# Optimization experiments

Hardware: AMD Instinct MI355X
Metric: run time of the kernel (lower is better)

## Reference

```python
import jax, jax.numpy as jnp
import numpy as np

B = 8192
NUM_SAMPLES = 128
RESAMPLE_PADDING = 0.01
F32_EPS = float(np.finfo(np.float32).eps)


def lift_gaussian_diag(d, t_mean, t_var, r_var):
    # d: [B,3]; t_mean/t_var/r_var: [B,S]
    mean = d[..., None, :] * t_mean[..., None]                      # [B,S,3]
    d_mag_sq = jnp.clip(jnp.sum(d ** 2, axis=-1, keepdims=True), 1e-10)
    d_outer_diag = d ** 2
    null_outer_diag = 1.0 - d_outer_diag / d_mag_sq
    cov_diag = (t_var[..., None] * d_outer_diag[..., None, :]
                + r_var[..., None] * null_outer_diag[..., None, :])  # [B,S,3]
    return mean, cov_diag


def conical_frustum_to_gaussian(d, t0, t1, base_radius):
    # stable=True branch of the original code
    mu = (t0 + t1) / 2
    hw = (t1 - t0) / 2
    t_mean = mu + 2 * mu * hw ** 2 / (3 * mu ** 2 + hw ** 2)
    t_var = hw ** 2 / 3 - 4 / 15 * (hw ** 4 * (12 * mu ** 2 - hw ** 2)
                                    / (3 * mu ** 2 + hw ** 2) ** 2)
    r_var = base_radius ** 2 * (mu ** 2 / 4 + 5 / 12 * hw ** 2
                                - 4 / 15 * hw ** 4 / (3 * mu ** 2 + hw ** 2))
    return lift_gaussian_diag(d, t_mean, t_var, r_var)


def cast_rays(t_vals, origins, directions, radii):
    # ray_shape == 'cone', diag == True
    means, covs = conical_frustum_to_gaussian(
        directions, t_vals[..., :-1], t_vals[..., 1:], radii)
    return means + origins[..., None, :], covs


def sorted_piecewise_constant_pdf(bins, weights, num_samples):
    # randomized=False branch; faithful O(n*m) mask-based interval search
    eps = 1e-5
    weight_sum = jnp.sum(weights, axis=-1, keepdims=True)
    padding = jnp.clip(eps - weight_sum, 0)
    weights = weights + padding / weights.shape[-1]
    weight_sum = weight_sum + padding
    pdf = weights / weight_sum
    cdf = jnp.minimum(jnp.cumsum(pdf[..., :-1], axis=-1), 1.0)
    z = jnp.zeros(cdf.shape[:-1] + (1,), cdf.dtype)
    o = jnp.ones(cdf.shape[:-1] + (1,), cdf.dtype)
    cdf = jnp.concatenate([z, cdf, o], axis=-1)                      # [B, nb+1]
    u = jnp.linspace(0.0, 1.0 - F32_EPS, num_samples, dtype=cdf.dtype)
    u = jnp.broadcast_to(u, cdf.shape[:-1] + (num_samples,))         # [B, S]
    mask = u[..., None, :] >= cdf[..., :, None]                      # [B, nb+1, S]

    def find_interval(x):
        x0 = jnp.max(jnp.where(mask, x[..., None], x[..., :1, None]), axis=-2)
        x1 = jnp.min(jnp.where(~mask, x[..., None], x[..., -1:, None]), axis=-2)
        return x0, x1

    bins_g0, bins_g1 = find_interval(bins)
    cdf_g0, cdf_g1 = find_interval(cdf)
    t = jnp.clip(jnp.nan_to_num((u - cdf_g0) / (cdf_g1 - cdf_g0)), 0, 1)
    return bins_g0 + t * (bins_g1 - bins_g0)


def setup_inputs() -> dict:
    key = jax.random.key(0)
    k0, k1, k2, k3 = jax.random.split(key, 4)
    origins = jax.random.normal(k0, (B, 3), dtype=jnp.float32)
    directions = jax.random.normal(k1, (B, 3), dtype=jnp.float32)
    directions = directions / jnp.linalg.norm(directions, axis=-1, keepdims=True)
    radii = 0.001 + 0.01 * jax.random.uniform(k2, (B, 1), dtype=jnp.float32)
    near = 2.0 * jnp.ones((B, 1), dtype=jnp.float32)
    far = 6.0 * jnp.ones((B, 1), dtype=jnp.float32)
    weights = jax.random.uniform(k3, (B, NUM_SAMPLES), dtype=jnp.float32)
    return {"origins": origins, "directions": directions, "radii": radii,
            "near": near, "far": far, "weights": weights}


def reference(origins, directions, radii, near, far, weights):
    # coarse stratified sampling (randomized=False, lindisp=False)
    t = jnp.linspace(0.0, 1.0, NUM_SAMPLES + 1, dtype=jnp.float32)
    t_coarse = near * (1.0 - t) + far * t                            # [B, S+1]
    means_c, covs_c = cast_rays(t_coarse, origins, directions, radii)
    # resample_along_rays: blur weights then inverse-CDF sample
    wpad = jnp.concatenate([weights[..., :1], weights, weights[..., -1:]], axis=-1)
    wmax = jnp.maximum(wpad[..., :-1], wpad[..., 1:])
    wblur = 0.5 * (wmax[..., :-1] + wmax[..., 1:]) + RESAMPLE_PADDING
    t_fine = sorted_piecewise_constant_pdf(t_coarse, wblur, t_coarse.shape[-1])
    means_f, covs_f = cast_rays(t_fine, origins, directions, radii)
    return (t_coarse, means_c, covs_c, t_fine, means_f, covs_f)
```

## Files before the change

### kernel.cpp

```cpp
#include <hip/hip_runtime.h>


constexpr int B_RAYS = 8192;
constexpr int S      = 128;
constexpr int SP1    = 129;
constexpr float F32_EPS = 1.1920928955078125e-07f;

constexpr long long O_TC = 0;
constexpr long long O_MC = O_TC + (long long)B_RAYS * SP1;
constexpr long long O_CC = O_MC + (long long)B_RAYS * S * 3;
constexpr long long O_TF = O_CC + (long long)B_RAYS * S * 3;
constexpr long long O_MF = O_TF + (long long)B_RAYS * SP1;
constexpr long long O_CF = O_MF + (long long)B_RAYS * S * 3;

__device__ __forceinline__ float frcp(float x) { return __builtin_amdgcn_rcpf(x); }

__device__ __forceinline__ void frustum(float t0, float t1, float rad2,
                                        float& tm, float& tv, float& rv)
{
    float mu  = 0.5f * (t0 + t1);
    float hw  = 0.5f * (t1 - t0);
    float mu2 = mu * mu, hw2 = hw * hw, hw4 = hw2 * hw2;
    float den  = fmaf(3.0f, mu2, hw2);
    float rden = frcp(den);
    tm = fmaf(2.0f * mu * hw2, rden, mu);
    tv = hw2 * (1.0f / 3.0f)
       - (4.0f / 15.0f) * (hw4 * fmaf(12.0f, mu2, -hw2)) * (rden * rden);
    rv = rad2 * (0.25f * mu2 + (5.0f / 12.0f) * hw2 - (4.0f / 15.0f) * hw4 * rden);
}

__device__ __forceinline__ float sel3(int c, float x, float y, float z)
{
    return (c == 0) ? x : ((c == 1) ? y : z);
}

__global__ __launch_bounds__(256) void mipnerf_kernel(
    const float* __restrict__ origins,
    const float* __restrict__ directions,
    const float* __restrict__ radii,
    const float* __restrict__ nearp,
    const float* __restrict__ farp,
    const float* __restrict__ weights,
    float* __restrict__ out)
{
    const int tid = threadIdx.x;
    const int w   = tid >> 6;
    const int l   = tid & 63;
    const int b   = (blockIdx.x << 2) + w;

    __shared__ float2 s_ft[4][128];
    __shared__ float  s_rv[4][128];
    __shared__ float  s_cdf[4][132];
    __shared__ float  s_tf[4][132];

    const float2 wv = *reinterpret_cast<const float2*>(weights + (long long)b * S + 2*l);
    const float ox = origins[3*b+0], oy = origins[3*b+1], oz = origins[3*b+2];
    const float dx = directions[3*b+0], dy = directions[3*b+1], dz = directions[3*b+2];
    const float rad = radii[b];
    const float nv = nearp[b], fv = farp[b];

    const float rad2   = rad * rad;
    const float axx = dx*dx, ayy = dy*dy, azz = dz*dz;
    const float dmag2  = fmaxf(axx + ayy + azz, 1e-10f);
    const float rdmag2 = frcp(dmag2);
    const float nxx = 1.0f - axx * rdmag2;
    const float nyy = 1.0f - ayy * rdmag2;
    const float nzz = 1.0f - azz * rdmag2;

    auto bin = [&](int k) {
        float t = (float)k * (1.0f / 128.0f);
        return nv * (1.0f - t) + fv * t;
    };

    {
        float* ot = out + O_TC + (long long)b * SP1;
        ot[l]      = bin(l);
        ot[l + 64] = bin(l + 64);
        if (l == 0) ot[128] = bin(128);
    }

    #pragma unroll
    for (int j = 0; j < 2; ++j) {
        int i = l + 64*j;
        float tm, tv, rv;
        frustum(bin(i), bin(i + 1), rad2, tm, tv, rv);
        s_ft[w][i] = make_float2(tm, tv);
        s_rv[w][i] = rv;
    }
    __builtin_amdgcn_wave_barrier();

    auto emit_span = [&](int m, float* __restrict__ om, float* __restrict__ oc) {
        int k0 = m + m / 3;
        int r  = 4*m - 3*k0;
        float2 fA = s_ft[w][k0], fB = s_ft[w][k0 + 1];
        float  rA = s_rv[w][k0], rB = s_rv[w][k0 + 1];
        float4 mv, cv;
        #pragma unroll
        for (int e = 0; e < 4; ++e) {
            int  rc   = r + e;
            bool useB = rc >= 3;
            int  c    = useB ? rc - 3 : rc;
            float tm = useB ? fB.x : fA.x;
            float tv = useB ? fB.y : fA.y;
            float rv = useB ? rB   : rA;
            (&mv.x)[e] = sel3(c, dx, dy, dz) * tm + sel3(c, ox, oy, oz);
            (&cv.x)[e] = tv * sel3(c, axx, ayy, azz) + rv * sel3(c, nxx, nyy, nzz);
        }
        *reinterpret_cast<float4*>(om + 4*m) = mv;
        *reinterpret_cast<float4*>(oc + 4*m) = cv;
    };

    {
        float* om = out + O_MC + (long long)b * 384;
        float* oc = out + O_CC + (long long)b * 384;
        emit_span(l, om, oc);
        if (l < 32) emit_span(l + 64, om, oc);
    }

    float wprev = __shfl_up(wv.y, 1);   if (l == 0)  wprev = wv.x;
    float wnext = __shfl_down(wv.x, 1); if (l == 63) wnext = wv.y;
    float m0 = fmaxf(wprev, wv.x), m1 = fmaxf(wv.x, wv.y), m2 = fmaxf(wv.y, wnext);
    float wb0 = 0.5f * (m0 + m1) + 0.01f;
    float wb1 = 0.5f * (m1 + m2) + 0.01f;

    float ps   = wb0 + wb1;
    float incl = ps;
    #pragma unroll
    for (int off = 1; off < 64; off <<= 1) {
        float y = __shfl_up(incl, off);
        if (l >= off) incl += y;
    }
    float total = __shfl(incl, 63);
    float pad   = fmaxf(1e-5f - total, 0.0f);
    float wstot = total + pad;
    float inv   = frcp(wstot);
    float padk  = pad * (1.0f / 128.0f);
    float excl  = incl - ps;

    float c1 = fminf((excl + wb0 + (float)(2*l + 1) * padk) * inv, 1.0f);
    float c2 = fminf((incl        + (float)(2*l + 2) * padk) * inv, 1.0f);
    s_cdf[w][2*l + 1] = c1;
    s_cdf[w][2*l + 2] = (l == 63) ? 1.0f : c2;
    if (l == 0) s_cdf[w][0] = 0.0f;
    __builtin_amdgcn_wave_barrier();

    const float ustep = (1.0f - F32_EPS) * (1.0f / 128.0f);
    const float u0 = (float)l * ustep;
    const float u1 = (float)(l + 64) * ustep;
    const float u2 = 128.0f * ustep;
    int lo0 = 0, hi0 = 128, lo1 = 0, hi1 = 128, lo2 = 0, hi2 = 128;
    #pragma unroll
    for (int it = 0; it < 7; ++it) {
        int q0 = (lo0 + hi0) >> 1, q1 = (lo1 + hi1) >> 1, q2 = (lo2 + hi2) >> 1;
        float a0 = s_cdf[w][q0], a1 = s_cdf[w][q1], a2 = s_cdf[w][q2];
        if (a0 <= u0) lo0 = q0; else hi0 = q0;
        if (a1 <= u1) lo1 = q1; else hi1 = q1;
        if (a2 <= u2) lo2 = q2; else hi2 = q2;
    }
    auto interp = [&](float u, int lo) {
        float c0  = s_cdf[w][lo], cg1 = s_cdf[w][lo + 1];
        float tt  = (u - c0) * frcp(cg1 - c0);
        if (!(tt == tt)) tt = 0.0f;
        tt = fminf(fmaxf(tt, 0.0f), 1.0f);
        float b0 = bin(lo);
        return fmaf(tt, bin(lo + 1) - b0, b0);
    };
    float tf0 = interp(u0, lo0);
    float tf1 = interp(u1, lo1);
    float tf2 = interp(u2, lo2);
    {
        float* ot = out + O_TF + (long long)b * SP1;
        s_tf[w][l]      = tf0;  ot[l]      = tf0;
        s_tf[w][l + 64] = tf1;  ot[l + 64] = tf1;
        if (l == 0) { s_tf[w][128] = tf2; ot[128] = tf2; }
    }
    __builtin_amdgcn_wave_barrier();

    #pragma unroll
    for (int j = 0; j < 2; ++j) {
        int i = l + 64*j;
        float tm, tv, rv;
        frustum(s_tf[w][i], s_tf[w][i + 1], rad2, tm, tv, rv);
        s_ft[w][i] = make_float2(tm, tv);
        s_rv[w][i] = rv;
    }
    __builtin_amdgcn_wave_barrier();

    {
        float* om = out + O_MF + (long long)b * 384;
        float* oc = out + O_CF + (long long)b * 384;
        emit_span(l, om, oc);
        if (l < 32) emit_span(l + 64, om, oc);
    }
}

extern "C" void kernel_launch(void* const* d_in, const int* in_sizes, int n_in,
                              void* d_out, int out_size, void* d_ws, size_t ws_size,
                              hipStream_t stream)
{
    const float* origins    = (const float*)d_in[0];
    const float* directions = (const float*)d_in[1];
    const float* radii      = (const float*)d_in[2];
    const float* nearp      = (const float*)d_in[3];
    const float* farp       = (const float*)d_in[4];
    const float* weights    = (const float*)d_in[5];
    float* out = (float*)d_out;

    mipnerf_kernel<<<B_RAYS / 4, 256, 0, stream>>>(
        origins, directions, radii, nearp, farp, weights, out);
}
```

Measured before the change: 17.95 us.

## Replace binary CDF search with scatter of interval payloads and DPP scans

Each CDF segment computes which uniform sample indices fall in it and writes a packed payload (cdf start, width, bin endpoints) into shared memory, so each sample reads one entry instead of running a 7-step binary search. The wave shuffles and prefix scan are swapped for DPP row operations plus readlane. Fine-frustum neighbours now come from DPP instead of a shared tf buffer, and the launch becomes one 64-thread block per ray with float4-packed frustum data. The risks are edge cases in the float rounding of the sample-index bounds, uneven scatter loop lengths across lanes, and the launch overhead of many small blocks.

```diff
diff --git a/kernel.cpp b/kernel.cpp
--- a/kernel.cpp
+++ b/kernel.cpp
@@ -5,6 +5,8 @@
 constexpr int S      = 128;
 constexpr int SP1    = 129;
 constexpr float F32_EPS = 1.1920928955078125e-07f;
+constexpr float USTEP   = (1.0f - F32_EPS) / 128.0f;
+constexpr float R_SCALE = 128.0f / (1.0f - F32_EPS);
 
 constexpr long long O_TC = 0;
 constexpr long long O_MC = O_TC + (long long)B_RAYS * SP1;
@@ -14,6 +16,19 @@
 constexpr long long O_CF = O_MF + (long long)B_RAYS * S * 3;
 
 __device__ __forceinline__ float frcp(float x) { return __builtin_amdgcn_rcpf(x); }
+
+template<int CTRL, int RM>
+__device__ __forceinline__ float dpp_addf(float x) {
+    int m = __builtin_amdgcn_update_dpp(0, __builtin_bit_cast(int, x),
+                                        CTRL, RM, 0xF, true);
+    return x + __builtin_bit_cast(float, m);
+}
+template<int CTRL>
+__device__ __forceinline__ float dpp_movf(float x) {
+    int m = __builtin_amdgcn_update_dpp(0, __builtin_bit_cast(int, x),
+                                        CTRL, 0xF, 0xF, true);
+    return __builtin_bit_cast(float, m);
+}
 
 __device__ __forceinline__ void frustum(float t0, float t1, float rad2,
                                         float& tm, float& tv, float& rv)
@@ -34,7 +49,20 @@
     return (c == 0) ? x : ((c == 1) ? y : z);
 }
 
-__global__ __launch_bounds__(256) void mipnerf_kernel(
+__device__ __forceinline__ int smin_of(float c)
+{
+    int s = (int)ceilf(c * R_SCALE);
+    s = s < 0 ? 0 : (s > 129 ? 129 : s);
+    #pragma unroll
+    for (int it = 0; it < 2; ++it)
+        if (s > 0 && (float)(s - 1) * USTEP >= c) --s;
+    #pragma unroll
+    for (int it = 0; it < 2; ++it)
+        if (s < 129 && (float)s * USTEP < c) ++s;
+    return s;
+}
+
+__global__ __launch_bounds__(64) void mipnerf_kernel(
     const float* __restrict__ origins,
     const float* __restrict__ directions,
     const float* __restrict__ radii,
@@ -43,15 +71,11 @@
     const float* __restrict__ weights,
     float* __restrict__ out)
 {
-    const int tid = threadIdx.x;
-    const int w   = tid >> 6;
-    const int l   = tid & 63;
-    const int b   = (blockIdx.x << 2) + w;
-
-    __shared__ float2 s_ft[4][128];
-    __shared__ float  s_rv[4][128];
-    __shared__ float  s_cdf[4][132];
-    __shared__ float  s_tf[4][132];
+    const int l = threadIdx.x;
+    const int b = blockIdx.x;
+
+    __shared__ float4 s_pay[132];
+    __shared__ float4 s_fr[128];
 
     const float2 wv = *reinterpret_cast<const float2*>(weights + (long long)b * S + 2*l);
     const float ox = origins[3*b+0], oy = origins[3*b+1], oz = origins[3*b+2];
@@ -84,16 +108,14 @@
         int i = l + 64*j;
         float tm, tv, rv;
         frustum(bin(i), bin(i + 1), rad2, tm, tv, rv);
-        s_ft[w][i] = make_float2(tm, tv);
-        s_rv[w][i] = rv;
+        s_fr[i] = make_float4(tm, tv, rv, 0.0f);
     }
     __builtin_amdgcn_wave_barrier();
 
     auto emit_span = [&](int m, float* __restrict__ om, float* __restrict__ oc) {
         int k0 = m + m / 3;
         int r  = 4*m - 3*k0;
-        float2 fA = s_ft[w][k0], fB = s_ft[w][k0 + 1];
-        float  rA = s_rv[w][k0], rB = s_rv[w][k0 + 1];
+        float4 fA = s_fr[k0], fB = s_fr[k0 + 1];
         float4 mv, cv;
         #pragma unroll
         for (int e = 0; e < 4; ++e) {
@@ -102,7 +124,7 @@
             int  c    = useB ? rc - 3 : rc;
             float tm = useB ? fB.x : fA.x;
             float tv = useB ? fB.y : fA.y;
-            float rv = useB ? rB   : rA;
+            float rv = useB ? fB.z : fA.z;
             (&mv.x)[e] = sel3(c, dx, dy, dz) * tm + sel3(c, ox, oy, oz);
             (&cv.x)[e] = tv * sel3(c, axx, ayy, azz) + rv * sel3(c, nxx, nyy, nzz);
         }
@@ -117,72 +139,74 @@
         if (l < 32) emit_span(l + 64, om, oc);
     }
 
-    float wprev = __shfl_up(wv.y, 1);   if (l == 0)  wprev = wv.x;
-    float wnext = __shfl_down(wv.x, 1); if (l == 63) wnext = wv.y;
+    float wprev = dpp_movf<0x138>(wv.y);  if (l == 0)  wprev = wv.x;
+    float wnext = dpp_movf<0x130>(wv.x);  if (l == 63) wnext = wv.y;
     float m0 = fmaxf(wprev, wv.x), m1 = fmaxf(wv.x, wv.y), m2 = fmaxf(wv.y, wnext);
     float wb0 = 0.5f * (m0 + m1) + 0.01f;
     float wb1 = 0.5f * (m1 + m2) + 0.01f;
 
-    float ps   = wb0 + wb1;
-    float incl = ps;
-    #pragma unroll
-    for (int off = 1; off < 64; off <<= 1) {
-        float y = __shfl_up(incl, off);
-        if (l >= off) incl += y;
-    }
-    float total = __shfl(incl, 63);
+    float ps = wb0 + wb1;
+    float x  = ps;
+    x = dpp_addf<0x111, 0xF>(x);
+    x = dpp_addf<0x112, 0xF>(x);
+    x = dpp_addf<0x114, 0xF>(x);
+    x = dpp_addf<0x118, 0xF>(x);
+    x = dpp_addf<0x142, 0xA>(x);
+    x = dpp_addf<0x143, 0xC>(x);
+    float incl  = x;
+    float total = __builtin_bit_cast(float,
+        __builtin_amdgcn_readlane(__builtin_bit_cast(int, incl), 63));
+
     float pad   = fmaxf(1e-5f - total, 0.0f);
     float wstot = total + pad;
     float inv   = frcp(wstot);
     float padk  = pad * (1.0f / 128.0f);
     float excl  = incl - ps;
 
-    float c1 = fminf((excl + wb0 + (float)(2*l + 1) * padk) * inv, 1.0f);
-    float c2 = fminf((incl        + (float)(2*l + 2) * padk) * inv, 1.0f);
-    s_cdf[w][2*l + 1] = c1;
-    s_cdf[w][2*l + 2] = (l == 63) ? 1.0f : c2;
-    if (l == 0) s_cdf[w][0] = 0.0f;
+    float Bv = fminf((excl + wb0 + (float)(2*l + 1) * padk) * inv, 1.0f);
+    float Cv = (l == 63) ? 1.0f
+             : fminf((incl + (float)(2*l + 2) * padk) * inv, 1.0f);
+    float Av = dpp_movf<0x138>(Cv);
+
+    int sm0 = smin_of(Av);
+    int sm1 = smin_of(Bv);
+    int sm2 = smin_of(Cv);
+    {
+        float4 payA = make_float4(Av, Bv - Av, bin(2*l),     bin(2*l + 1));
+        float4 payB = make_float4(Bv, Cv - Bv, bin(2*l + 1), bin(2*l + 2));
+        for (int s2 = sm0; s2 < sm1; ++s2) s_pay[s2] = payA;
+        for (int s2 = sm1; s2 < sm2; ++s2) s_pay[s2] = payB;
+    }
     __builtin_amdgcn_wave_barrier();
 
-    const float ustep = (1.0f - F32_EPS) * (1.0f / 128.0f);
-    const float u0 = (float)l * ustep;
-    const float u1 = (float)(l + 64) * ustep;
-    const float u2 = 128.0f * ustep;
-    int lo0 = 0, hi0 = 128, lo1 = 0, hi1 = 128, lo2 = 0, hi2 = 128;
-    #pragma unroll
-    for (int it = 0; it < 7; ++it) {
-        int q0 = (lo0 + hi0) >> 1, q1 = (lo1 + hi1) >> 1, q2 = (lo2 + hi2) >> 1;
-        float a0 = s_cdf[w][q0], a1 = s_cdf[w][q1], a2 = s_cdf[w][q2];
-        if (a0 <= u0) lo0 = q0; else hi0 = q0;
-        if (a1 <= u1) lo1 = q1; else hi1 = q1;
-        if (a2 <= u2) lo2 = q2; else hi2 = q2;
-    }
-    auto interp = [&](float u, int lo) {
-        float c0  = s_cdf[w][lo], cg1 = s_cdf[w][lo + 1];
-        float tt  = (u - c0) * frcp(cg1 - c0);
+    auto sample_one = [&](int s) -> float {
+        float4 p = s_pay[s];
+        float u  = (float)s * USTEP;
+        float tt = (u - p.x) * frcp(p.y);
         if (!(tt == tt)) tt = 0.0f;
         tt = fminf(fmaxf(tt, 0.0f), 1.0f);
-        float b0 = bin(lo);
-        return fmaf(tt, bin(lo + 1) - b0, b0);
+        return p.z + tt * (p.w - p.z);
     };
-    float tf0 = interp(u0, lo0);
-    float tf1 = interp(u1, lo1);
-    float tf2 = interp(u2, lo2);
+    float tf0 = sample_one(l);
+    float tf1 = sample_one(l + 64);
+    float tf2 = sample_one(128);
     {
         float* ot = out + O_TF + (long long)b * SP1;
-        s_tf[w][l]      = tf0;  ot[l]      = tf0;
-        s_tf[w][l + 64] = tf1;  ot[l + 64] = tf1;
-        if (l == 0) { s_tf[w][128] = tf2; ot[128] = tf2; }
-    }
-    __builtin_amdgcn_wave_barrier();
-
-    #pragma unroll
-    for (int j = 0; j < 2; ++j) {
-        int i = l + 64*j;
+        ot[l]      = tf0;
+        ot[l + 64] = tf1;
+        if (l == 0) ot[128] = tf2;
+    }
+
+    float tf1_0 = __builtin_bit_cast(float,
+        __builtin_amdgcn_readfirstlane(__builtin_bit_cast(int, tf1)));
+    float tA1 = dpp_movf<0x130>(tf0);  if (l == 63) tA1 = tf1_0;
+    float tB1 = dpp_movf<0x130>(tf1);  if (l == 63) tB1 = tf2;
+    {
         float tm, tv, rv;
-        frustum(s_tf[w][i], s_tf[w][i + 1], rad2, tm, tv, rv);
-        s_ft[w][i] = make_float2(tm, tv);
-        s_rv[w][i] = rv;
+        frustum(tf0, tA1, rad2, tm, tv, rv);
+        s_fr[l] = make_float4(tm, tv, rv, 0.0f);
+        frustum(tf1, tB1, rad2, tm, tv, rv);
+        s_fr[l + 64] = make_float4(tm, tv, rv, 0.0f);
     }
     __builtin_amdgcn_wave_barrier();
 
@@ -206,6 +230,6 @@
     const float* weights    = (const float*)d_in[5];
     float* out = (float*)d_out;
 
-    mipnerf_kernel<<<B_RAYS / 4, 256, 0, stream>>>(
+    mipnerf_kernel<<<B_RAYS, 64, 0, stream>>>(
         origins, directions, radii, nearp, farp, weights, out);
 }
```

Measured after the change: 17.79 us. No clear change (-0.9%).
